# Optimization experiments

Measured on AMD Instinct MI355X. Metric: run time of the kernel, lower is better.

## Reference

```python
import jax, jax.numpy as jnp
import numpy as np

N_CRYST = 256
ATOMS_PER = 64
N_ATOMS = N_CRYST * ATOMS_PER          # 16384
N_EDGES = N_ATOMS * 20                 # 327680 (max_neighbors=20)
HID = 128                              # hidden_dim / emb_size_atom / emb_size_edge
LAT = 256                              # latent_dim
NRAD = 128                             # radial basis size
NBLOCK = 3                             # interaction blocks
MAXZ = 100                             # MAX_ATOMIC_NUM
CUTOFF = 6.0


def lattice_matrix(lengths, angles):
    """CDVAE lattice_params_to_matrix: (B,3),(B,3 deg) -> (B,3,3)."""
    a, b, c = lengths[:, 0], lengths[:, 1], lengths[:, 2]
    al, be, ga = (jnp.deg2rad(angles[:, i]) for i in range(3))
    cos_a, cos_b, cos_g = jnp.cos(al), jnp.cos(be), jnp.cos(ga)
    sin_a, sin_b = jnp.sin(al), jnp.sin(be)
    val = jnp.clip((cos_a * cos_b - cos_g) / (sin_a * sin_b), -1.0, 1.0)
    gs = jnp.arccos(val)  # gamma*
    zero = jnp.zeros_like(a)
    va = jnp.stack([a * sin_b, zero, a * cos_b], -1)
    vb = jnp.stack([-b * sin_a * jnp.cos(gs), b * sin_a * jnp.sin(gs), b * cos_a], -1)
    vc = jnp.stack([zero, zero, c], -1)
    return jnp.stack([va, vb, vc], 1)


def setup_inputs() -> dict:
    key = jax.random.key(0)
    ks = jax.random.split(key, 20)
    p = lambda k, shp: jax.random.normal(k, shp, jnp.float32) * 0.05
    inp = {
        "z": jax.random.normal(ks[0], (N_CRYST, LAT), jnp.float32),
        "pred_frac_coords": jax.random.uniform(ks[1], (N_ATOMS, 3), jnp.float32),
        "pred_atom_types": jax.random.randint(ks[2], (N_ATOMS,), 0, MAXZ),
        "num_atoms": jnp.full((N_CRYST,), ATOMS_PER, jnp.int32),
        "lengths": 5.0 + 5.0 * jax.random.uniform(ks[3], (N_CRYST, 3), jnp.float32),
        "angles": 60.0 + 60.0 * jax.random.uniform(ks[4], (N_CRYST, 3), jnp.float32),
        "edge_index": jax.random.randint(ks[5], (2, N_EDGES), 0, N_ATOMS),
        # learned parameters
        "atom_emb": p(ks[6], (MAXZ, HID)),
        "W_in": p(ks[7], (HID + LAT, HID)), "b_in": jnp.zeros((HID,), jnp.float32),
        "W_rbf": p(ks[8], (NRAD, HID)),
        "W_edge": p(ks[9], (3 * HID, HID)), "b_edge": jnp.zeros((HID,), jnp.float32),
        "W_msg": p(ks[10], (NBLOCK, HID, HID)), "b_msg": jnp.zeros((NBLOCK, HID), jnp.float32),
        "W_gate": p(ks[11], (NBLOCK, HID, HID)),
        "W_upd": p(ks[12], (NBLOCK, HID, HID)), "b_upd": jnp.zeros((NBLOCK, HID), jnp.float32),
        "W_force": p(ks[13], (HID, 1)),
        "W_atom": p(ks[14], (HID, MAXZ)), "b_atom": jnp.zeros((MAXZ,), jnp.float32),
    }
    return inp


def reference(z, pred_frac_coords, pred_atom_types, num_atoms, lengths, angles,
              edge_index, atom_emb, W_in, b_in, W_rbf, W_edge, b_edge,
              W_msg, b_msg, W_gate, W_upd, b_upd, W_force, W_atom, b_atom):
    silu = jax.nn.silu
    batch = jnp.arange(N_ATOMS) // ATOMS_PER  # atom -> crystal (uniform 64 atoms/crystal)

    # fractional -> cartesian using per-crystal lattice
    latt = lattice_matrix(lengths, angles)                       # (B,3,3)
    cart = jnp.einsum("ni,nij->nj", pred_frac_coords, latt[batch])  # (N,3)

    src, dst = edge_index[0], edge_index[1]
    vec = cart[dst] - cart[src]                                   # (E,3)
    d = jnp.linalg.norm(vec, axis=-1) + 1e-8                      # (E,)
    unit = vec / d[:, None]

    # radial basis with smooth cosine envelope
    centers = jnp.linspace(0.0, CUTOFF, NRAD)
    width = CUTOFF / NRAD
    env = 0.5 * (jnp.cos(jnp.pi * jnp.clip(d / CUTOFF, 0.0, 1.0)) + 1.0)
    rbf = jnp.exp(-((d[:, None] - centers) ** 2) / (2.0 * width * width)) * env[:, None]
    rbf_h = rbf @ W_rbf                                           # (E,HID)

    # atom embedding conditioned on latent z (broadcast per crystal)
    h = silu(jnp.concatenate([atom_emb[pred_atom_types], z[batch]], -1) @ W_in + b_in)

    # edge embedding
    m = silu(jnp.concatenate([h[src], h[dst], rbf_h], -1) @ W_edge + b_edge)  # (E,HID)

    # interaction blocks: edge message update, rbf gating, scatter to atoms
    for i in range(NBLOCK):
        m2 = silu(m @ W_msg[i] + b_msg[i]) * (rbf_h @ W_gate[i])
        agg = jax.ops.segment_sum(m2, dst, num_segments=N_ATOMS)  # (N,HID)
        h = h + silu(agg @ W_upd[i] + b_upd[i])
        m = m + m2

    # per-edge force scalar -> cartesian coord diff per atom
    f_edge = (m @ W_force) * unit                                 # (E,3)
    pred_cart_coord_diff = jax.ops.segment_sum(f_edge, dst, num_segments=N_ATOMS)

    pred_atom_types_out = h @ W_atom + b_atom                     # (N,MAXZ)
    return (pred_cart_coord_diff, pred_atom_types_out)
```

## Files before the change

### kernel.cpp

```cpp
#include <hip/hip_runtime.h>
#include <hip/hip_bf16.h>

#define N_CRYST 256
#define ATOMS_PER 64
#define N_ATOMS (N_CRYST * ATOMS_PER)
#define N_EDGES (N_ATOMS * 20)
#define HID 128
#define LAT 256
#define NRAD 128
#define NBLOCK 3
#define MAXZ 100
#define CUTOFF 6.0f
#define PI_F 3.14159265358979323846f
#define ETILE 64
#define TABN 2048

typedef unsigned short ushort_t;
typedef unsigned char uchar_t;
typedef unsigned long long ull_t;
typedef __attribute__((ext_vector_type(8))) short short8;
typedef __attribute__((ext_vector_type(4))) float f32x4;

__device__ __forceinline__ float fexp2(float x) {
    float r; asm("v_exp_f32 %0, %1" : "=v"(r) : "v"(x)); return r;
}
__device__ __forceinline__ float frcp(float x) {
    float r; asm("v_rcp_f32 %0, %1" : "=v"(r) : "v"(x)); return r;
}
__device__ __forceinline__ float silu(float x) {
    return x * frcp(1.0f + fexp2(x * -1.44269504f));
}

__device__ __forceinline__ ushort_t f2bf(float v) {
    unsigned int u = __float_as_uint(v);
    return (ushort_t)((u + 0x7FFF + ((u >> 16) & 1)) >> 16);
}
__device__ __forceinline__ float bf2f(ushort_t u) {
    return __uint_as_float((unsigned int)u << 16);
}

__device__ __forceinline__ f32x4 MFMA(short8 a, short8 b, f32x4 c) {
    return __builtin_amdgcn_mfma_f32_16x16x32_bf16(a, b, c, 0, 0, 0);
}

__device__ __forceinline__ int swz(int row, int k) {
    return (row * 256 + k * 2) ^ ((row & 7) << 4);
}
__device__ __forceinline__ int swzT(int col, int e) {
    return (col * 128 + e * 2) ^ ((col & 7) << 4);
}

__device__ __forceinline__ short8 ldB(const ushort_t* W, int col, int K, int k) {
    return *reinterpret_cast<const short8*>(W + (size_t)col * K + k);
}

__global__ void k_init(float* __restrict__ out, float* __restrict__ agg,
                       int* __restrict__ cnt) {
    int i = blockIdx.x * blockDim.x + threadIdx.x;
    if (i < N_ATOMS * 3) out[i] = 0.0f;
    if (i < N_ATOMS) cnt[i] = 0;
    if (i < NBLOCK * N_ATOMS * HID) agg[i] = 0.0f;
}

__global__ void k_hist(const int* __restrict__ edge_index, int* __restrict__ cnt) {
    int e = blockIdx.x * blockDim.x + threadIdx.x;
    if (e < N_EDGES) atomicAdd(&cnt[edge_index[N_EDGES + e]], 1);
}

__global__ void k_scan(const int* __restrict__ cnt, int* __restrict__ cursor) {
    __shared__ int partial[256];
    int t = threadIdx.x;
    int base = t * (N_ATOMS / 256);
    int s = 0;
    for (int j = 0; j < N_ATOMS / 256; j++) s += cnt[base + j];
    partial[t] = s;
    __syncthreads();
    if (t == 0) {
        int run = 0;
        for (int i = 0; i < 256; i++) { int v = partial[i]; partial[i] = run; run += v; }
    }
    __syncthreads();
    int run = partial[t];
    for (int j = 0; j < N_ATOMS / 256; j++) {
        cursor[base + j] = run;
        run += cnt[base + j];
    }
}

__global__ void k_scatter(const int* __restrict__ edge_index,
                          int* __restrict__ cursor, int* __restrict__ perm) {
    int e = blockIdx.x * blockDim.x + threadIdx.x;
    if (e < N_EDGES) {
        int pos = atomicAdd(&cursor[edge_index[N_EDGES + e]], 1);
        perm[pos] = e;
    }
}

__global__ void k_latt(const float* __restrict__ lengths,
                       const float* __restrict__ angles,
                       float* __restrict__ latt) {
    int c = blockIdx.x * blockDim.x + threadIdx.x;
    if (c >= N_CRYST) return;
    float a  = lengths[c * 3 + 0];
    float b  = lengths[c * 3 + 1];
    float cc = lengths[c * 3 + 2];
    float al = angles[c * 3 + 0] * (PI_F / 180.0f);
    float be = angles[c * 3 + 1] * (PI_F / 180.0f);
    float ga = angles[c * 3 + 2] * (PI_F / 180.0f);
    float cos_a = cosf(al), cos_b = cosf(be), cos_g = cosf(ga);
    float sin_a = sinf(al), sin_b = sinf(be);
    float val = (cos_a * cos_b - cos_g) / (sin_a * sin_b);
    val = fminf(1.0f, fmaxf(-1.0f, val));
    float gs = acosf(val);
    float* L = latt + c * 9;
    L[0] = a * sin_b;              L[1] = 0.0f;                  L[2] = a * cos_b;
    L[3] = -b * sin_a * cosf(gs);  L[4] = b * sin_a * sinf(gs);  L[5] = b * cos_a;
    L[6] = 0.0f;                   L[7] = 0.0f;                  L[8] = cc;
}

__global__ void k_cart(const float* __restrict__ frac,
                       const float* __restrict__ latt,
                       float* __restrict__ cart) {
    int n = blockIdx.x * blockDim.x + threadIdx.x;
    if (n >= N_ATOMS) return;
    int b = n / ATOMS_PER;
    const float* L = latt + b * 9;
    float f0 = frac[n * 3 + 0], f1 = frac[n * 3 + 1], f2 = frac[n * 3 + 2];
    cart[n * 3 + 0] = f0 * L[0] + f1 * L[3] + f2 * L[6];
    cart[n * 3 + 1] = f0 * L[1] + f1 * L[4] + f2 * L[7];
    cart[n * 3 + 2] = f0 * L[2] + f1 * L[5] + f2 * L[8];
}

__global__ void k_tab(const float* __restrict__ W_rbf, float* __restrict__ T) {
    int j = blockIdx.x;
    int c = threadIdx.x;
    __shared__ float rbf[NRAD];
    float d = (float)j * (CUTOFF / TABN);
    const float inv2w2 = 1.0f / (2.0f * (CUTOFF / NRAD) * (CUTOFF / NRAD));
    const float cstep = CUTOFF / (NRAD - 1);
    float x = fminf(1.0f, d * (1.0f / CUTOFF));
    float env = 0.5f * (cosf(PI_F * x) + 1.0f);
    float diff = d - (float)c * cstep;
    rbf[c] = expf(-diff * diff * inv2w2) * env;
    __syncthreads();
    float acc = 0.0f;
#pragma unroll 8
    for (int k = 0; k < NRAD; k++) acc += rbf[k] * W_rbf[k * HID + c];
    T[j * HID + c] = acc;
}

__global__ void k_prep(const float* __restrict__ W_edge,
                       const float* __restrict__ W_msg,
                       const float* __restrict__ W_gate,
                       const float* __restrict__ W_upd,
                       const float* __restrict__ W_atom,
                       ushort_t* __restrict__ Wt_edge,
                       ushort_t* __restrict__ Wt_msg,
                       ushort_t* __restrict__ Wt_gate,
                       ushort_t* __restrict__ Wt_upd,
                       ushort_t* __restrict__ Wt_atom) {
    int i = blockIdx.x * blockDim.x + threadIdx.x;
    if (i < 128 * 384) {
        int c = i / 384, k = i % 384;
        Wt_edge[(size_t)c * 384 + k] = f2bf(W_edge[k * 128 + c]);
    }
    if (i < 3 * 128 * 128) {
        int blk = i >> 14, r = i & 16383;
        int c = r >> 7, k = r & 127;
        Wt_msg[blk * 16384 + c * 128 + k]  = f2bf(W_msg[blk * 16384 + k * 128 + c]);
        Wt_gate[blk * 16384 + c * 128 + k] = f2bf(W_gate[blk * 16384 + k * 128 + c]);
        Wt_upd[blk * 16384 + c * 128 + k]  = f2bf(W_upd[blk * 16384 + k * 128 + c]);
    }
    if (i < 128 * 128) {
        int c = i >> 7, k = i & 127;
        Wt_atom[c * 128 + k] = (c < MAXZ) ? f2bf(W_atom[k * MAXZ + c]) : (ushort_t)0;
    }
}

__global__ void k_embW(const float* __restrict__ atom_emb,
                       const float* __restrict__ W_in,
                       const float* __restrict__ b_in,
                       float* __restrict__ embW) {
    int zi = blockIdx.x;
    int c = threadIdx.x;
    __shared__ float row[HID];
    row[c] = atom_emb[zi * HID + c];
    __syncthreads();
    float acc = b_in[c];
#pragma unroll 8
    for (int k = 0; k < HID; k++) acc += row[k] * W_in[k * HID + c];
    embW[zi * HID + c] = acc;
}

__global__ void k_zW(const float* __restrict__ z,
                     const float* __restrict__ W_in,
                     float* __restrict__ zW) {
    int b = blockIdx.x;
    int c = threadIdx.x;
    __shared__ float row[LAT];
    row[c]       = z[b * LAT + c];
    row[128 + c] = z[b * LAT + 128 + c];
    __syncthreads();
    float acc = 0.f;
#pragma unroll 8
    for (int k = 0; k < LAT; k++) acc += row[k] * W_in[(HID + k) * HID + c];
    zW[b * HID + c] = acc;
}

__global__ void k_h2(const int* __restrict__ types,
                     const float* __restrict__ embW,
                     const float* __restrict__ zW,
                     ushort_t* __restrict__ h_bf) {
    int idx = blockIdx.x * 256 + threadIdx.x;
    int n = idx >> 7, c = idx & 127;
    float v = embW[types[n] * HID + c] + zW[(n >> 6) * HID + c];
    h_bf[idx] = f2bf(silu(v));
}

__global__ __launch_bounds__(256)
void k_edges(const int* __restrict__ perm,
             const int* __restrict__ edge_index,
             const float* __restrict__ cart,
             const float* __restrict__ T,
             const ushort_t* __restrict__ h_bf,
             const ushort_t* __restrict__ Wt_edge,
             const float* __restrict__ b_edge,
             const ushort_t* __restrict__ Wt_msg,
             const float* __restrict__ b_msg,
             const ushort_t* __restrict__ Wt_gate,
             const float* __restrict__ W_force,
             float* __restrict__ agg,
             float* __restrict__ outF)
{
    __shared__ ushort_t R2[ETILE * HID];
    __shared__ ushort_t R3[ETILE * HID];
    __shared__ ushort_t M2T[HID * ETILE];
    __shared__ int   sm_src[ETILE], sm_dst[ETILE];
    __shared__ float sm_unit[ETILE][3];
    __shared__ float sm_d[ETILE];
    __shared__ float sm_f[ETILE];
    __shared__ uchar_t sm_runid8[ETILE];
    __shared__ int   sm_slotdst[ETILE];
    __shared__ int   sm_nruns;

    const int t    = threadIdx.x;
    const int lane = t & 63;
    const int wave = t >> 6;
    const int l15  = lane & 15;
    const int g4   = lane >> 4;
    const int lk8  = 8 * g4;
    const int colw = wave * 32;
    const int e0   = blockIdx.x * ETILE;

    const int laneA = l15 * 256 + ((lk8 * 2) ^ ((l15 & 7) << 4));
    int woff[2][4];
#pragma unroll
    for (int nt = 0; nt < 2; nt++)
#pragma unroll
        for (int r = 0; r < 4; r++) {
            int row = g4 * 4 + r;
            woff[nt][r] = row * 256 + (((colw + nt * 16 + l15) * 2) ^ ((row & 7) << 4));
        }

    if (t < ETILE) {
        int e = t;
        int eid = perm[e0 + e];
        int s = edge_index[eid];
        int d = edge_index[N_EDGES + eid];
        sm_src[e] = s; sm_dst[e] = d;
        float vx = cart[d * 3 + 0] - cart[s * 3 + 0];
        float vy = cart[d * 3 + 1] - cart[s * 3 + 1];
        float vz = cart[d * 3 + 2] - cart[s * 3 + 2];
        float dist = sqrtf(vx * vx + vy * vy + vz * vz) + 1e-8f;
        sm_d[e] = dist;
        float di = 1.0f / dist;
        sm_unit[e][0] = vx * di; sm_unit[e][1] = vy * di; sm_unit[e][2] = vz * di;
        sm_f[e] = 0.0f;
    }
    __syncthreads();

    if (wave == 0) {
        int e = lane;
        int d = sm_dst[e];
        int prev = (e == 0) ? -1 : sm_dst[e - 1];
        ull_t mask = __ballot(d != prev);
        int rid = __popcll(mask & ((2ull << e) - 1)) - 1;
        sm_runid8[e] = (uchar_t)rid;
        if (d != prev) sm_slotdst[rid] = d;
        if (e == 0) sm_nruns = __popcll(mask);
    }

    {
#pragma unroll
        for (int it = 0; it < 8; it++) {
            int u = it * 256 + t;
            int e = u >> 5;
            int p = u & 31;
            float idxf = sm_d[e] * (TABN / CUTOFF);
            idxf = fminf(idxf, (float)TABN);
            int j = (int)idxf;
            float fr = idxf - (float)j;
            f32x4 lo = *reinterpret_cast<const f32x4*>(T + (size_t)j * HID + 4 * p);
            f32x4 hi = *reinterpret_cast<const f32x4*>(T + (size_t)(j + 1) * HID + 4 * p);
            unsigned int pk0, pk1;
            {
                float v0 = lo[0] + fr * (hi[0] - lo[0]);
                float v1 = lo[1] + fr * (hi[1] - lo[1]);
                float v2 = lo[2] + fr * (hi[2] - lo[2]);
                float v3 = lo[3] + fr * (hi[3] - lo[3]);
                pk0 = ((unsigned int)f2bf(v1) << 16) | f2bf(v0);
                pk1 = ((unsigned int)f2bf(v3) << 16) | f2bf(v2);
            }
            int off = (e * 256 + 8 * p) ^ ((e & 7) << 4);
            *reinterpret_cast<unsigned int*>(reinterpret_cast<char*>(R2) + off)     = pk0;
            *reinterpret_cast<unsigned int*>(reinterpret_cast<char*>(R2) + off + 4) = pk1;
        }
    }
    __syncthreads();

    int srcr[4], dstr[4];
#pragma unroll
    for (int at = 0; at < 4; at++) {
        srcr[at] = sm_src[at * 16 + l15];
        dstr[at] = sm_dst[at * 16 + l15];
    }

    float m_acc[4][2][4];
    {
        f32x4 am[4][2];
#pragma unroll
        for (int at = 0; at < 4; at++)
#pragma unroll
            for (int nt = 0; nt < 2; nt++)
                am[at][nt] = (f32x4){0.f, 0.f, 0.f, 0.f};
#pragma unroll
        for (int seg = 0; seg < 3; seg++) {
#pragma unroll
            for (int ks = 0; ks < 4; ks++) {
                int kg = seg * 128 + ks * 32 + lk8;
                short8 B0 = ldB(Wt_edge, colw + l15,      384, kg);
                short8 B1 = ldB(Wt_edge, colw + 16 + l15, 384, kg);
#pragma unroll
                for (int at = 0; at < 4; at++) {
                    short8 A;
                    if (seg == 0)
                        A = *reinterpret_cast<const short8*>(
                            h_bf + (size_t)srcr[at] * HID + ks * 32 + lk8);
                    else if (seg == 1)
                        A = *reinterpret_cast<const short8*>(
                            h_bf + (size_t)dstr[at] * HID + ks * 32 + lk8);
                    else
                        A = *reinterpret_cast<const short8*>(
                            reinterpret_cast<const char*>(R2) + ((laneA ^ (ks * 64)) + at * 4096));
                    am[at][0] = MFMA(A, B0, am[at][0]);
                    am[at][1] = MFMA(A, B1, am[at][1]);
                }
            }
        }
        float be0 = b_edge[colw + l15];
        float be1 = b_edge[colw + 16 + l15];
#pragma unroll
        for (int at = 0; at < 4; at++)
#pragma unroll
            for (int r = 0; r < 4; r++) {
                m_acc[at][0][r] = silu(am[at][0][r] + be0);
                m_acc[at][1][r] = silu(am[at][1][r] + be1);
            }
#pragma unroll
        for (int at = 0; at < 4; at++)
#pragma unroll
            for (int nt = 0; nt < 2; nt++)
#pragma unroll
                for (int r = 0; r < 4; r++)
                    *reinterpret_cast<ushort_t*>(reinterpret_cast<char*>(R3) +
                        (woff[nt][r] + at * 4096)) = f2bf(m_acc[at][nt][r]);
    }
    __syncthreads();

    for (int i = 0; i < NBLOCK; i++) {
        const ushort_t* Wm = Wt_msg  + i * 16384;
        const ushort_t* Wg = Wt_gate + i * 16384;
        float* aggp = agg + (size_t)i * N_ATOMS * HID;
#pragma unroll
        for (int nt = 0; nt < 2; nt++) {
            int col = colw + nt * 16 + l15;
            float bm = b_msg[i * HID + col];
            f32x4 am_[4], ag_[4];
#pragma unroll
            for (int at = 0; at < 4; at++) {
                am_[at] = (f32x4){0.f, 0.f, 0.f, 0.f};
                ag_[at] = (f32x4){0.f, 0.f, 0.f, 0.f};
            }
#pragma unroll
            for (int ks = 0; ks < 4; ks++) {
                short8 Bm = ldB(Wm, col, 128, ks * 32 + lk8);
                short8 Bg = ldB(Wg, col, 128, ks * 32 + lk8);
                int lA = laneA ^ (ks * 64);
#pragma unroll
                for (int at = 0; at < 4; at++) {
                    short8 Am = *reinterpret_cast<const short8*>(
                        reinterpret_cast<const char*>(R3) + (lA + at * 4096));
                    short8 Ag = *reinterpret_cast<const short8*>(
                        reinterpret_cast<const char*>(R2) + (lA + at * 4096));
                    am_[at] = MFMA(Am, Bm, am_[at]);
                    ag_[at] = MFMA(Ag, Bg, ag_[at]);
                }
            }
#pragma unroll
            for (int at = 0; at < 4; at++) {
                float m2v[4];
#pragma unroll
                for (int r = 0; r < 4; r++) {
                    float m2 = silu(am_[at][r] + bm) * ag_[at][r];
                    m2v[r] = m2;
                    m_acc[at][nt][r] += m2;
                }
                unsigned int plo = ((unsigned int)f2bf(m2v[1]) << 16) | f2bf(m2v[0]);
                unsigned int phi = ((unsigned int)f2bf(m2v[3]) << 16) | f2bf(m2v[2]);
                ull_t pk = ((ull_t)phi << 32) | plo;
                int addr = (col * 128 + (at * 16 + g4 * 4) * 2) ^ ((col & 7) << 4);
                *reinterpret_cast<ull_t*>(reinterpret_cast<char*>(M2T) + addr) = pk;
            }
        }
        __syncthreads();

        {
            int nruns = sm_nruns;
            short8 Bm2[2][2];
#pragma unroll
            for (int ct = 0; ct < 2; ct++)
#pragma unroll
                for (int ks = 0; ks < 2; ks++) {
                    int col = colw + ct * 16 + l15;
                    int addr = (col * 128 + (ks * 32 + lk8) * 2) ^ ((col & 7) << 4);
                    Bm2[ct][ks] = *reinterpret_cast<const short8*>(
                        reinterpret_cast<const char*>(M2T) + addr);
                }
            for (int rt = 0; rt * 16 < nruns; rt++) {
                int tv = l15 + rt * 16;
                short8 SA[2];
#pragma unroll
                for (int ks = 0; ks < 2; ks++) {
                    ull_t rid8 = *reinterpret_cast<const ull_t*>(sm_runid8 + ks * 32 + lk8);
                    unsigned int rlo = (unsigned int)rid8;
                    unsigned int rhi = (unsigned int)(rid8 >> 32);
                    union { unsigned int u[4]; short8 s8; } sb;
#pragma unroll
                    for (int q = 0; q < 2; q++) {
                        unsigned int rr = q ? rhi : rlo;
                        unsigned int w0 = 0, w1 = 0;
                        if ((int)((rr >>  0) & 255) == tv) w0 |= 0x3F80u;
                        if ((int)((rr >>  8) & 255) == tv) w0 |= 0x3F800000u;
                        if ((int)((rr >> 16) & 255) == tv) w1 |= 0x3F80u;
                        if ((int)((rr >> 24) & 255) == tv) w1 |= 0x3F800000u;
                        sb.u[q * 2]     = w0;
                        sb.u[q * 2 + 1] = w1;
                    }
                    SA[ks] = sb.s8;
                }
                f32x4 acc0 = {0.f, 0.f, 0.f, 0.f}, acc1 = {0.f, 0.f, 0.f, 0.f};
                acc0 = MFMA(SA[0], Bm2[0][0], acc0);
                acc0 = MFMA(SA[1], Bm2[0][1], acc0);
                acc1 = MFMA(SA[0], Bm2[1][0], acc1);
                acc1 = MFMA(SA[1], Bm2[1][1], acc1);
#pragma unroll
                for (int r = 0; r < 4; r++) {
                    int run = rt * 16 + g4 * 4 + r;
                    if (run < nruns) {
                        int d = sm_slotdst[run];
                        atomicAdd(&aggp[(size_t)d * HID + colw + l15],      acc0[r]);
                        atomicAdd(&aggp[(size_t)d * HID + colw + 16 + l15], acc1[r]);
                    }
                }
            }
        }

        if (i < NBLOCK - 1) {
#pragma unroll
            for (int at = 0; at < 4; at++)
#pragma unroll
                for (int nt = 0; nt < 2; nt++)
#pragma unroll
                    for (int r = 0; r < 4; r++)
                        *reinterpret_cast<ushort_t*>(reinterpret_cast<char*>(R3) +
                            (woff[nt][r] + at * 4096)) = f2bf(m_acc[at][nt][r]);
        }
        __syncthreads();
    }

    {
        float wf0 = W_force[colw + l15];
        float wf1 = W_force[colw + 16 + l15];
#pragma unroll
        for (int at = 0; at < 4; at++)
#pragma unroll
            for (int r = 0; r < 4; r++) {
                float part = m_acc[at][0][r] * wf0 + m_acc[at][1][r] * wf1;
                part += __shfl_xor(part, 1, 64);
                part += __shfl_xor(part, 2, 64);
                part += __shfl_xor(part, 4, 64);
                part += __shfl_xor(part, 8, 64);
                if (l15 == 0)
                    atomicAdd(&sm_f[at * 16 + g4 * 4 + r], part);
            }
        __syncthreads();
        if (t < ETILE) {
            int e = t;
            int d = sm_dst[e];
            if (e == 0 || sm_dst[e - 1] != d) {
                float fx = 0.f, fy = 0.f, fz = 0.f;
                int j = e;
                do {
                    float f = sm_f[j];
                    fx += f * sm_unit[j][0];
                    fy += f * sm_unit[j][1];
                    fz += f * sm_unit[j][2];
                    j++;
                } while (j < ETILE && sm_dst[j] == d);
                atomicAdd(&outF[d * 3 + 0], fx);
                atomicAdd(&outF[d * 3 + 1], fy);
                atomicAdd(&outF[d * 3 + 2], fz);
            }
        }
    }
}

__global__ __launch_bounds__(256)
void k_atom2(const float* __restrict__ agg,
             const ushort_t* __restrict__ Wt_upd,
             const float* __restrict__ b_upd,
             const ushort_t* __restrict__ Wt_atom,
             const float* __restrict__ b_atom,
             const ushort_t* __restrict__ h_bf,
             float* __restrict__ out) {
    __shared__ ushort_t RA[64 * HID];

    const int t    = threadIdx.x;
    const int lane = t & 63;
    const int wave = t >> 6;
    const int l15  = lane & 15;
    const int lk8  = 8 * (lane >> 4);
    const int colw = wave * 32;
    const int n0   = blockIdx.x * 64;

    const int laneA = l15 * 256 + ((lk8 * 2) ^ ((l15 & 7) << 4));
    int woff[2][4];
#pragma unroll
    for (int nt = 0; nt < 2; nt++)
#pragma unroll
        for (int r = 0; r < 4; r++) {
            int row = (lane >> 4) * 4 + r;
            woff[nt][r] = row * 256 + (((colw + nt * 16 + l15) * 2) ^ ((row & 7) << 4));
        }

    float h_acc[4][2][4];
#pragma unroll
    for (int at = 0; at < 4; at++)
#pragma unroll
        for (int nt = 0; nt < 2; nt++)
#pragma unroll
            for (int r = 0; r < 4; r++) {
                int row = at * 16 + (lane >> 4) * 4 + r;
                h_acc[at][nt][r] = bf2f(h_bf[(size_t)(n0 + row) * HID + colw + nt * 16 + l15]);
            }

    for (int i = 0; i < NBLOCK; i++) {
        const float* ap = agg + (size_t)i * N_ATOMS * HID + (size_t)n0 * HID;
#pragma unroll
        for (int it = 0; it < 8; it++) {
            int u = it * 256 + t;
            int row = u >> 5, p = u & 31;
            f32x4 v = *reinterpret_cast<const f32x4*>(ap + (size_t)row * HID + 4 * p);
            unsigned int pk0 = ((unsigned int)f2bf(v[1]) << 16) | f2bf(v[0]);
            unsigned int pk1 = ((unsigned int)f2bf(v[3]) << 16) | f2bf(v[2]);
            int off = (row * 256 + 8 * p) ^ ((row & 7) << 4);
            *reinterpret_cast<unsigned int*>(reinterpret_cast<char*>(RA) + off)     = pk0;
            *reinterpret_cast<unsigned int*>(reinterpret_cast<char*>(RA) + off + 4) = pk1;
        }
        __syncthreads();

        const ushort_t* Wu = Wt_upd + i * 16384;
        float bu0 = b_upd[i * HID + colw + l15];
        float bu1 = b_upd[i * HID + colw + 16 + l15];
        f32x4 am[4][2];
#pragma unroll
        for (int at = 0; at < 4; at++)
#pragma unroll
            for (int nt = 0; nt < 2; nt++)
                am[at][nt] = (f32x4){0.f, 0.f, 0.f, 0.f};
#pragma unroll
        for (int ks = 0; ks < 4; ks++) {
            short8 B0 = ldB(Wu, colw + l15,      128, ks * 32 + lk8);
            short8 B1 = ldB(Wu, colw + 16 + l15, 128, ks * 32 + lk8);
            int lA = laneA ^ (ks * 64);
#pragma unroll
            for (int at = 0; at < 4; at++) {
                short8 A = *reinterpret_cast<const short8*>(
                    reinterpret_cast<const char*>(RA) + (lA + at * 4096));
                am[at][0] = MFMA(A, B0, am[at][0]);
                am[at][1] = MFMA(A, B1, am[at][1]);
            }
        }
#pragma unroll
        for (int at = 0; at < 4; at++)
#pragma unroll
            for (int r = 0; r < 4; r++) {
                h_acc[at][0][r] += silu(am[at][0][r] + bu0);
                h_acc[at][1][r] += silu(am[at][1][r] + bu1);
            }
        __syncthreads();
    }

#pragma unroll
    for (int at = 0; at < 4; at++)
#pragma unroll
        for (int nt = 0; nt < 2; nt++)
#pragma unroll
            for (int r = 0; r < 4; r++)
                *reinterpret_cast<ushort_t*>(reinterpret_cast<char*>(RA) +
                    (woff[nt][r] + at * 4096)) = f2bf(h_acc[at][nt][r]);
    __syncthreads();

    {
        f32x4 am[4][2];
#pragma unroll
        for (int at = 0; at < 4; at++)
#pragma unroll
            for (int nt = 0; nt < 2; nt++)
                am[at][nt] = (f32x4){0.f, 0.f, 0.f, 0.f};
#pragma unroll
        for (int ks = 0; ks < 4; ks++) {
            short8 B0 = ldB(Wt_atom, colw + l15,      128, ks * 32 + lk8);
            short8 B1 = ldB(Wt_atom, colw + 16 + l15, 128, ks * 32 + lk8);
            int lA = laneA ^ (ks * 64);
#pragma unroll
            for (int at = 0; at < 4; at++) {
                short8 A = *reinterpret_cast<const short8*>(
                    reinterpret_cast<const char*>(RA) + (lA + at * 4096));
                am[at][0] = MFMA(A, B0, am[at][0]);
                am[at][1] = MFMA(A, B1, am[at][1]);
            }
        }
        int col0 = colw + l15;
        int col1 = colw + 16 + l15;
        float ba0 = (col0 < MAXZ) ? b_atom[col0] : 0.f;
        float ba1 = (col1 < MAXZ) ? b_atom[col1] : 0.f;
#pragma unroll
        for (int at = 0; at < 4; at++)
#pragma unroll
            for (int r = 0; r < 4; r++) {
                int row = n0 + at * 16 + (lane >> 4) * 4 + r;
                if (col0 < MAXZ)
                    out[(size_t)N_ATOMS * 3 + (size_t)row * MAXZ + col0] = am[at][0][r] + ba0;
                if (col1 < MAXZ)
                    out[(size_t)N_ATOMS * 3 + (size_t)row * MAXZ + col1] = am[at][1][r] + ba1;
            }
    }
}

extern "C" void kernel_launch(void* const* d_in, const int* in_sizes, int n_in,
                              void* d_out, int out_size, void* d_ws, size_t ws_size,
                              hipStream_t stream) {
    const float* z         = (const float*)d_in[0];
    const float* frac      = (const float*)d_in[1];
    const int*   types     = (const int*)d_in[2];
    const float* lengths   = (const float*)d_in[4];
    const float* angles    = (const float*)d_in[5];
    const int*   edge_idx  = (const int*)d_in[6];
    const float* atom_emb  = (const float*)d_in[7];
    const float* W_in      = (const float*)d_in[8];
    const float* b_in      = (const float*)d_in[9];
    const float* W_rbf     = (const float*)d_in[10];
    const float* W_edge    = (const float*)d_in[11];
    const float* b_edge    = (const float*)d_in[12];
    const float* W_msg     = (const float*)d_in[13];
    const float* b_msg     = (const float*)d_in[14];
    const float* W_gate    = (const float*)d_in[15];
    const float* W_upd     = (const float*)d_in[16];
    const float* b_upd     = (const float*)d_in[17];
    const float* W_force   = (const float*)d_in[18];
    const float* W_atom    = (const float*)d_in[19];
    const float* b_atom    = (const float*)d_in[20];

    float* out = (float*)d_out;

    float* ws = (float*)d_ws;
    size_t off = 0;
    float* latt = ws + off; off += N_CRYST * 9;
    float* cart = ws + off; off += (size_t)N_ATOMS * 3;
    float* agg  = ws + off; off += (size_t)NBLOCK * N_ATOMS * HID;
    float* embW = ws + off; off += MAXZ * HID;
    float* zW   = ws + off; off += N_CRYST * HID;
    float* T    = ws + off; off += (size_t)(TABN + 2) * HID;
    int* cnt    = (int*)(ws + off); off += N_ATOMS;
    int* cursor = (int*)(ws + off); off += N_ATOMS;
    int* perm   = (int*)(ws + off); off += N_EDGES;
    off = (off + 7) & ~(size_t)7;
    ushort_t* ub = (ushort_t*)(ws + off);
    size_t uoff = 0;
    ushort_t* h_bf    = ub + uoff; uoff += (size_t)N_ATOMS * HID;
    ushort_t* Wt_edge = ub + uoff; uoff += 128 * 384;
    ushort_t* Wt_msg  = ub + uoff; uoff += 3 * 128 * 128;
    ushort_t* Wt_gate = ub + uoff; uoff += 3 * 128 * 128;
    ushort_t* Wt_upd  = ub + uoff; uoff += 3 * 128 * 128;
    ushort_t* Wt_atom = ub + uoff; uoff += 128 * 128;

    k_init<<<(NBLOCK * N_ATOMS * HID + 255) / 256, 256, 0, stream>>>(out, agg, cnt);

    k_hist<<<(N_EDGES + 255) / 256, 256, 0, stream>>>(edge_idx, cnt);
    k_scan<<<1, 256, 0, stream>>>(cnt, cursor);
    k_scatter<<<(N_EDGES + 255) / 256, 256, 0, stream>>>(edge_idx, cursor, perm);

    k_latt<<<1, 256, 0, stream>>>(lengths, angles, latt);
    k_cart<<<(N_ATOMS + 255) / 256, 256, 0, stream>>>(frac, latt, cart);
    k_tab<<<TABN + 2, HID, 0, stream>>>(W_rbf, T);
    k_prep<<<192, 256, 0, stream>>>(W_edge, W_msg, W_gate, W_upd, W_atom,
                                    Wt_edge, Wt_msg, Wt_gate, Wt_upd, Wt_atom);

    k_embW<<<MAXZ, HID, 0, stream>>>(atom_emb, W_in, b_in, embW);
    k_zW<<<N_CRYST, HID, 0, stream>>>(z, W_in, zW);
    k_h2<<<(N_ATOMS * HID) / 256, 256, 0, stream>>>(types, embW, zW, h_bf);

    k_edges<<<N_EDGES / ETILE, 256, 0, stream>>>(perm, edge_idx, cart, T, h_bf,
                                                 Wt_edge, b_edge,
                                                 Wt_msg, b_msg, Wt_gate, W_force,
                                                 agg, out);

    k_atom2<<<N_ATOMS / 64, 256, 0, stream>>>(agg, Wt_upd, b_upd, Wt_atom, b_atom,
                                              h_bf, out);
}
```

Before: 450.8 us.

## Split edge kernel output columns across eight waves instead of four

The edge kernel now runs 512 threads per block, and each wave owns 16 output columns instead of 32. This halves per-thread accumulator state and per-wave MFMA work while keeping the same 64-edge tile and shared-memory staging. Launch bounds now request 4 blocks per CU, aiming for more resident waves and better latency hiding. The cost is more waves issuing the same A-tile LDS reads and more barrier participants per block.

```diff
diff --git a/kernel.cpp b/kernel.cpp
--- a/kernel.cpp
+++ b/kernel.cpp
@@ -45,9 +45,6 @@
 
 __device__ __forceinline__ int swz(int row, int k) {
     return (row * 256 + k * 2) ^ ((row & 7) << 4);
-}
-__device__ __forceinline__ int swzT(int col, int e) {
-    return (col * 128 + e * 2) ^ ((col & 7) << 4);
 }
 
 __device__ __forceinline__ short8 ldB(const ushort_t* W, int col, int K, int k) {
@@ -217,7 +214,7 @@
     h_bf[idx] = f2bf(silu(v));
 }
 
-__global__ __launch_bounds__(256)
+__global__ __launch_bounds__(512, 4)
 void k_edges(const int* __restrict__ perm,
              const int* __restrict__ edge_index,
              const float* __restrict__ cart,
@@ -249,18 +246,17 @@
     const int l15  = lane & 15;
     const int g4   = lane >> 4;
     const int lk8  = 8 * g4;
-    const int colw = wave * 32;
+    const int colw = wave * 16;
     const int e0   = blockIdx.x * ETILE;
 
     const int laneA = l15 * 256 + ((lk8 * 2) ^ ((l15 & 7) << 4));
-    int woff[2][4];
-#pragma unroll
-    for (int nt = 0; nt < 2; nt++)
-#pragma unroll
-        for (int r = 0; r < 4; r++) {
-            int row = g4 * 4 + r;
-            woff[nt][r] = row * 256 + (((colw + nt * 16 + l15) * 2) ^ ((row & 7) << 4));
-        }
+    const int colM  = colw + l15;
+    int woff[4];
+#pragma unroll
+    for (int r = 0; r < 4; r++) {
+        int row = g4 * 4 + r;
+        woff[r] = row * 256 + ((colM * 2) ^ ((row & 7) << 4));
+    }
 
     if (t < ETILE) {
         int e = t;
@@ -292,8 +288,8 @@
 
     {
 #pragma unroll
-        for (int it = 0; it < 8; it++) {
-            int u = it * 256 + t;
+        for (int it = 0; it < 4; it++) {
+            int u = it * 512 + t;
             int e = u >> 5;
             int p = u & 31;
             float idxf = sm_d[e] * (TABN / CUTOFF);
@@ -325,21 +321,17 @@
         dstr[at] = sm_dst[at * 16 + l15];
     }
 
-    float m_acc[4][2][4];
+    float m_acc[4][4];
     {
-        f32x4 am[4][2];
-#pragma unroll
-        for (int at = 0; at < 4; at++)
-#pragma unroll
-            for (int nt = 0; nt < 2; nt++)
-                am[at][nt] = (f32x4){0.f, 0.f, 0.f, 0.f};
+        f32x4 am[4];
+#pragma unroll
+        for (int at = 0; at < 4; at++) am[at] = (f32x4){0.f, 0.f, 0.f, 0.f};
 #pragma unroll
         for (int seg = 0; seg < 3; seg++) {
 #pragma unroll
             for (int ks = 0; ks < 4; ks++) {
                 int kg = seg * 128 + ks * 32 + lk8;
-                short8 B0 = ldB(Wt_edge, colw + l15,      384, kg);
-                short8 B1 = ldB(Wt_edge, colw + 16 + l15, 384, kg);
+                short8 B0 = ldB(Wt_edge, colM, 384, kg);
 #pragma unroll
                 for (int at = 0; at < 4; at++) {
                     short8 A;
@@ -352,28 +344,22 @@
                     else
                         A = *reinterpret_cast<const short8*>(
                             reinterpret_cast<const char*>(R2) + ((laneA ^ (ks * 64)) + at * 4096));
-                    am[at][0] = MFMA(A, B0, am[at][0]);
-                    am[at][1] = MFMA(A, B1, am[at][1]);
+                    am[at] = MFMA(A, B0, am[at]);
                 }
             }
         }
-        float be0 = b_edge[colw + l15];
-        float be1 = b_edge[colw + 16 + l15];
+        float be0 = b_edge[colM];
 #pragma unroll
         for (int at = 0; at < 4; at++)
 #pragma unroll
-            for (int r = 0; r < 4; r++) {
-                m_acc[at][0][r] = silu(am[at][0][r] + be0);
-                m_acc[at][1][r] = silu(am[at][1][r] + be1);
-            }
+            for (int r = 0; r < 4; r++)
+                m_acc[at][r] = silu(am[at][r] + be0);
 #pragma unroll
         for (int at = 0; at < 4; at++)
 #pragma unroll
-            for (int nt = 0; nt < 2; nt++)
-#pragma unroll
-                for (int r = 0; r < 4; r++)
-                    *reinterpret_cast<ushort_t*>(reinterpret_cast<char*>(R3) +
-                        (woff[nt][r] + at * 4096)) = f2bf(m_acc[at][nt][r]);
+            for (int r = 0; r < 4; r++)
+                *reinterpret_cast<ushort_t*>(reinterpret_cast<char*>(R3) +
+                    (woff[r] + at * 4096)) = f2bf(m_acc[at][r]);
     }
     __syncthreads();
 
@@ -381,10 +367,8 @@
         const ushort_t* Wm = Wt_msg  + i * 16384;
         const ushort_t* Wg = Wt_gate + i * 16384;
         float* aggp = agg + (size_t)i * N_ATOMS * HID;
-#pragma unroll
-        for (int nt = 0; nt < 2; nt++) {
-            int col = colw + nt * 16 + l15;
-            float bm = b_msg[i * HID + col];
+        {
+            float bm = b_msg[i * HID + colM];
             f32x4 am_[4], ag_[4];
 #pragma unroll
             for (int at = 0; at < 4; at++) {
@@ -393,8 +377,8 @@
             }
 #pragma unroll
             for (int ks = 0; ks < 4; ks++) {
-                short8 Bm = ldB(Wm, col, 128, ks * 32 + lk8);
-                short8 Bg = ldB(Wg, col, 128, ks * 32 + lk8);
+                short8 Bm = ldB(Wm, colM, 128, ks * 32 + lk8);
+                short8 Bg = ldB(Wg, colM, 128, ks * 32 + lk8);
                 int lA = laneA ^ (ks * 64);
 #pragma unroll
                 for (int at = 0; at < 4; at++) {
@@ -413,12 +397,12 @@
                 for (int r = 0; r < 4; r++) {
                     float m2 = silu(am_[at][r] + bm) * ag_[at][r];
                     m2v[r] = m2;
-                    m_acc[at][nt][r] += m2;
+                    m_acc[at][r] += m2;
                 }
                 unsigned int plo = ((unsigned int)f2bf(m2v[1]) << 16) | f2bf(m2v[0]);
                 unsigned int phi = ((unsigned int)f2bf(m2v[3]) << 16) | f2bf(m2v[2]);
                 ull_t pk = ((ull_t)phi << 32) | plo;
-                int addr = (col * 128 + (at * 16 + g4 * 4) * 2) ^ ((col & 7) << 4);
+                int addr = (colM * 128 + (at * 16 + g4 * 4) * 2) ^ ((colM & 7) << 4);
                 *reinterpret_cast<ull_t*>(reinterpret_cast<char*>(M2T) + addr) = pk;
             }
         }
@@ -426,16 +410,13 @@
 
         {
             int nruns = sm_nruns;
-            short8 Bm2[2][2];
-#pragma unroll
-            for (int ct = 0; ct < 2; ct++)
-#pragma unroll
-                for (int ks = 0; ks < 2; ks++) {
-                    int col = colw + ct * 16 + l15;
-                    int addr = (col * 128 + (ks * 32 + lk8) * 2) ^ ((col & 7) << 4);
-                    Bm2[ct][ks] = *reinterpret_cast<const short8*>(
-                        reinterpret_cast<const char*>(M2T) + addr);
-                }
+            short8 Bm2[2];
+#pragma unroll
+            for (int ks = 0; ks < 2; ks++) {
+                int addr = (colM * 128 + (ks * 32 + lk8) * 2) ^ ((colM & 7) << 4);
+                Bm2[ks] = *reinterpret_cast<const short8*>(
+                    reinterpret_cast<const char*>(M2T) + addr);
+            }
             for (int rt = 0; rt * 16 < nruns; rt++) {
                 int tv = l15 + rt * 16;
                 short8 SA[2];
@@ -458,18 +439,15 @@
                     }
                     SA[ks] = sb.s8;
                 }
-                f32x4 acc0 = {0.f, 0.f, 0.f, 0.f}, acc1 = {0.f, 0.f, 0.f, 0.f};
-                acc0 = MFMA(SA[0], Bm2[0][0], acc0);
-                acc0 = MFMA(SA[1], Bm2[0][1], acc0);
-                acc1 = MFMA(SA[0], Bm2[1][0], acc1);
-                acc1 = MFMA(SA[1], Bm2[1][1], acc1);
+                f32x4 acc0 = {0.f, 0.f, 0.f, 0.f};
+                acc0 = MFMA(SA[0], Bm2[0], acc0);
+                acc0 = MFMA(SA[1], Bm2[1], acc0);
 #pragma unroll
                 for (int r = 0; r < 4; r++) {
                     int run = rt * 16 + g4 * 4 + r;
                     if (run < nruns) {
                         int d = sm_slotdst[run];
-                        atomicAdd(&aggp[(size_t)d * HID + colw + l15],      acc0[r]);
-                        atomicAdd(&aggp[(size_t)d * HID + colw + 16 + l15], acc1[r]);
+                        atomicAdd(&aggp[(size_t)d * HID + colM], acc0[r]);
                     }
                 }
             }
@@ -479,23 +457,20 @@
 #pragma unroll
             for (int at = 0; at < 4; at++)
 #pragma unroll
-                for (int nt = 0; nt < 2; nt++)
-#pragma unroll
-                    for (int r = 0; r < 4; r++)
-                        *reinterpret_cast<ushort_t*>(reinterpret_cast<char*>(R3) +
-                            (woff[nt][r] + at * 4096)) = f2bf(m_acc[at][nt][r]);
+                for (int r = 0; r < 4; r++)
+                    *reinterpret_cast<ushort_t*>(reinterpret_cast<char*>(R3) +
+                        (woff[r] + at * 4096)) = f2bf(m_acc[at][r]);
         }
         __syncthreads();
     }
 
     {
-        float wf0 = W_force[colw + l15];
-        float wf1 = W_force[colw + 16 + l15];
+        float wf0 = W_force[colM];
 #pragma unroll
         for (int at = 0; at < 4; at++)
 #pragma unroll
             for (int r = 0; r < 4; r++) {
-                float part = m_acc[at][0][r] * wf0 + m_acc[at][1][r] * wf1;
+                float part = m_acc[at][r] * wf0;
                 part += __shfl_xor(part, 1, 64);
                 part += __shfl_xor(part, 2, 64);
                 part += __shfl_xor(part, 4, 64);
@@ -721,7 +696,7 @@
     k_zW<<<N_CRYST, HID, 0, stream>>>(z, W_in, zW);
     k_h2<<<(N_ATOMS * HID) / 256, 256, 0, stream>>>(types, embW, zW, h_bf);
 
-    k_edges<<<N_EDGES / ETILE, 256, 0, stream>>>(perm, edge_idx, cart, T, h_bf,
+    k_edges<<<N_EDGES / ETILE, 512, 0, stream>>>(perm, edge_idx, cart, T, h_bf,
                                                  Wt_edge, b_edge,
                                                  Wt_msg, b_msg, Wt_gate, W_force,
                                                  agg, out);
```

Result: slower. 463.0 us (+2.7%).
